# Optimization experiments

Hardware: AMD Instinct MI355X
Metric: run time of the kernel (lower is better)

Reference implementation:

```python
import jax, jax.numpy as jnp
import numpy as np
from jax import lax

B, CIN, COUT, H, W = 16, 320, 320, 64, 64
R, NUM_LORAS, LORA_STRIDE, SCALE, K = 4, 50, 4, 1.0, 3


def setup_inputs() -> dict:
    key = jax.random.key(0)
    k1, k2, k3, k4, k5, k6 = jax.random.split(key, 6)
    x = jax.random.normal(k1, (B, CIN, H, W), dtype=jnp.float32)
    lora_id = jax.random.randint(k2, (B,), 0, NUM_LORAS * LORA_STRIDE, dtype=jnp.int64)
    conv_w = jax.random.normal(k3, (COUT, CIN, K, K), dtype=jnp.float32) * (1.0 / np.sqrt(CIN * K * K))
    conv_b = jax.random.normal(k4, (COUT,), dtype=jnp.float32) * 0.01
    # stacked LoRA banks: down [L, r, Cin, 3, 3], up [L, Cout, r] (1x1 conv squeezed)
    down_w = jax.random.normal(k5, (NUM_LORAS, R, CIN, K, K), dtype=jnp.float32) * (1.0 / R)
    up_w = jax.random.normal(k6, (NUM_LORAS, COUT, R), dtype=jnp.float32) * 0.02
    return {"x": x, "conv_w": conv_w, "conv_b": conv_b, "down_w": down_w, "up_w": up_w, "lora_id": lora_id}


def _conv3x3(x, w):
    # x: [N, C, H, W], w: [O, C, 3, 3], stride 1, padding 1
    return lax.conv_general_dilated(x, w, (1, 1), [(1, 1), (1, 1)],
                                    dimension_numbers=("NCHW", "OIHW", "NCHW"))


def reference(x, conv_w, conv_b, down_w, up_w, lora_id):
    idx = lora_id // LORA_STRIDE                      # [B]
    active = (idx >= 0).astype(x.dtype)               # [B] mask; negative -> base conv only
    safe = jnp.clip(idx, 0, NUM_LORAS - 1)
    # base conv on full batch (dropout is identity at inference)
    base = _conv3x3(x, conv_w) + conv_b[None, :, None, None]  # [B, Cout, H, W]
    # per-sample gathered down conv (3x3), vmapped over batch (MoE-style dispatch)
    wd = down_w[safe]                                 # [B, r, Cin, 3, 3]
    down = jax.vmap(lambda xi, wi: _conv3x3(xi[None], wi)[0])(x, wd)  # [B, r, H, W]
    # per-sample 1x1 up conv as einsum with gathered up weights
    up = jnp.einsum("brhw,bor->bohw", down, up_w[safe])  # [B, Cout, H, W]
    return base + SCALE * up * active[:, None, None, None]
```

## Files before the change

kernel.cpp:

```cpp
#include <hip/hip_runtime.h>

typedef unsigned short ushort_t;
typedef unsigned int   uint_t;
typedef __attribute__((ext_vector_type(8))) short  short8;
typedef __attribute__((ext_vector_type(4))) float  float4v;
typedef __attribute__((ext_vector_type(4))) uint_t uint4v;
typedef __attribute__((ext_vector_type(2))) uint_t uint2v;

#define B_    16
#define CIN_  320
#define COUT_ 320
#define NLORA 50
#define R_    4
#define NCH   10

#define XCHUNK (66*66*32)
#define WCHUNK (9*COUT_*32)
#define DCHUNK (9*16*32)

#define WB16_OFF  44605440ULL
#define DWNE_OFF  46448640ULL
#define DOWN_OFF  47923200ULL

__device__ __forceinline__ ushort_t bf16rne(float f) {
  uint_t u = __float_as_uint(f);
  u = (u + 0x7FFFu + ((u >> 16) & 1u)) >> 16;
  return (ushort_t)u;
}

__device__ __forceinline__ void gld16(const ushort_t* g, ushort_t* l) {
  __builtin_amdgcn_global_load_lds(
      (const __attribute__((address_space(1))) void*)g,
      (__attribute__((address_space(3))) void*)l,
      16, 0, 0);
}

__device__ __forceinline__ void lora_idx(const void* lora, int b, int* l_out,
                                         float* act_out) {
  const int* p32 = (const int*)lora;
  bool odd0 = true;
  #pragma unroll
  for (int i = 1; i < 16; i += 2) odd0 = odd0 && (p32[i] == 0);
  long long raw = odd0 ? ((const long long*)lora)[b] : (long long)p32[b];
  long long idx = (raw >= 0) ? (raw >> 2) : -(((-raw) + 3) >> 2);
  *act_out = (idx >= 0) ? 1.0f : 0.0f;
  *l_out = (int)(idx < 0 ? 0 : (idx > (NLORA - 1) ? (NLORA - 1) : idx));
}

__global__ __launch_bounds__(256)
void pad_convert(const float* __restrict__ x, ushort_t* __restrict__ x_pad) {
  __shared__ float t[64][65];
  const int cc  = blockIdx.x;
  const int h   = blockIdx.y;
  const int b   = blockIdx.z;
  const int tid = threadIdx.x;
  #pragma unroll
  for (int it = 0; it < 4; ++it) {
    int idx = it * 256 + tid;
    int cl = idx >> 4, w4 = (idx & 15) * 4;
    float4v v = *(const float4v*)(x +
        (((size_t)(b * CIN_ + cc * 64 + cl)) * 64 + h) * 64 + w4);
    t[cl][w4] = v[0]; t[cl][w4 + 1] = v[1];
    t[cl][w4 + 2] = v[2]; t[cl][w4 + 3] = v[3];
  }
  __syncthreads();
  #pragma unroll
  for (int it = 0; it < 4; ++it) {
    int j  = it * 256 + tid;
    int cq = j & 15, wl = j >> 4;
    int cl = cq * 4;
    uint_t u0 = (uint_t)bf16rne(t[cl][wl])     | ((uint_t)bf16rne(t[cl + 1][wl]) << 16);
    uint_t u1 = (uint_t)bf16rne(t[cl + 2][wl]) | ((uint_t)bf16rne(t[cl + 3][wl]) << 16);
    int chunk = cc * 2 + (cl >> 5);
    uint2v u; u[0] = u0; u[1] = u1;
    *(uint2v*)(x_pad + (((size_t)(b * NCH + chunk) * 66 + (h + 1)) * 66 + (wl + 1)) * 32
               + (cl & 31)) = u;
  }
  if (h == 0) {
    #pragma unroll
    for (int s = 0; s < 2; ++s) {
      ushort_t* base = x_pad + (size_t)(b * NCH + cc * 2 + s) * XCHUNK;
      for (int g = tid; g < 528; g += 256) {
        int r = (g >= 264) ? 1 : 0;
        int g2 = g - r * 264;
        int col = g2 >> 2, qg = g2 & 3;
        *(uint4v*)(base + ((size_t)(r * 65) * 66 + col) * 32 + qg * 8) = (uint4v)0u;
      }
      for (int g = tid; g < 512; g += 256) {
        int row = 1 + (g >> 3);
        int col = ((g >> 2) & 1) * 65;
        int qg  = g & 3;
        *(uint4v*)(base + ((size_t)row * 66 + col) * 32 + qg * 8) = (uint4v)0u;
      }
    }
  }
}

__global__ __launch_bounds__(512)
void wconv(const float* __restrict__ conv_w, ushort_t* __restrict__ wb16) {
  int idx = blockIdx.x * 512 + threadIdx.x;
  int c5 = idx & 31;
  int o  = (idx >> 5) % COUT_;
  int rest = idx / (COUT_ * 32);
  int tap = rest % 9, chunk = rest / 9;
  wb16[idx] = bf16rne(conv_w[((size_t)o * CIN_ + chunk * 32 + c5) * 9 + tap]);
}

__global__ __launch_bounds__(512)
void dwnconv(const float* __restrict__ down_w, const void* __restrict__ lora,
             ushort_t* __restrict__ dwn_eff) {
  const int b = blockIdx.x;
  int l; float act;
  lora_idx(lora, b, &l, &act);
  ushort_t* dst = dwn_eff + (size_t)b * (NCH * DCHUNK);
  const float* src = down_w + (size_t)l * (R_ * CIN_ * 9);
  for (int it = 0; it < 90; ++it) {
    int idx = it * 512 + threadIdx.x;
    int c5 = idx & 31;
    int r  = (idx >> 5) & 15;
    int rest = idx >> 9;
    int tap = rest % 9, chunk = rest / 9;
    float v = (r < R_) ? act * src[((size_t)(r * CIN_) + chunk * 32 + c5) * 9 + tap]
                       : 0.0f;
    dst[idx] = bf16rne(v);
  }
}

#define LXG    1360
#define LXGP   1408
#define LWG    576
#define LTOTG  2048
#define LBUF_B (LTOTG * 16)

__global__ __launch_bounds__(512)
void lora_down(const ushort_t* __restrict__ x_pad, const ushort_t* __restrict__ dwn_eff,
               float* __restrict__ down) {
  __shared__ __align__(16) char smem[2 * LBUF_B];

  const int tid = threadIdx.x;
  const int lin = blockIdx.x;
  const int b   = lin >> 4;
  const int hw  = lin & 15;
  const int h0  = (hw & 7) * 8;
  const int w0  = (hw >> 3) * 32;

  const int wv = tid >> 6;
  const int la = tid & 15;
  const int q  = (tid >> 4) & 3;

  const ushort_t* psrc[4];
  int step[4];
  #pragma unroll
  for (int r = 0; r < 4; ++r) {
    int g = r * 512 + tid;
    if (g < LXGP) {
      int gx = (g < LXG) ? g : (LXG - 1);
      int qq = gx & 3, t = gx >> 2;
      int hh = t / 34, ww = t - hh * 34;
      psrc[r] = x_pad + (size_t)b * NCH * XCHUNK
              + (((h0 + hh) * 66 + (w0 + ww)) * 32 + (qq ^ ((ww >> 1) & 3)) * 8);
      step[r] = XCHUNK;
    } else {
      int gw = g - LXGP;
      if (gw > LWG - 1) gw = LWG - 1;
      int qq = gw & 3, t2 = gw >> 2;
      int rr = t2 & 15, tap = t2 >> 4;
      psrc[r] = dwn_eff + (size_t)b * NCH * DCHUNK
              + ((tap * 16 + rr) * 32 + (qq ^ ((rr >> 1) & 3)) * 8);
      step[r] = DCHUNK;
    }
  }

  const char* ax0[3]; const char* ax1[3];
  #pragma unroll
  for (int kw = 0; kw < 3; ++kw) {
    int base = (wv * 34 + la + kw) * 64 + (q ^ (((la + kw) >> 1) & 3)) * 16;
    ax0[kw] = smem + base;
    ax1[kw] = smem + LBUF_B + base;
  }
  const int bfb = 22528 + la * 64 + (q ^ ((la >> 1) & 3)) * 16;
  const char* aw0 = smem + bfb;
  const char* aw1 = smem + LBUF_B + bfb;

  float4v acc[2];
  acc[0] = (float4v)0.0f; acc[1] = (float4v)0.0f;

  auto STAGE = [&](int sel) {
    ushort_t* bufb = (ushort_t*)(smem + sel * LBUF_B);
    #pragma unroll
    for (int r = 0; r < 4; ++r) {
      gld16(psrc[r], bufb + (r * 512 + wv * 64) * 8);
      psrc[r] += step[r];
    }
  };

  auto PHASE = [&](const char* axA, const char* axB, const char* axC,
                   const char* aw, bool do_stage, int sel_next) {
    __builtin_amdgcn_s_barrier();
    if (do_stage) STAGE(sel_next);
    __builtin_amdgcn_sched_barrier(0);
    if (do_stage) asm volatile("s_waitcnt vmcnt(4)" ::: "memory");
    else          asm volatile("s_waitcnt vmcnt(0)" ::: "memory");
    __builtin_amdgcn_sched_barrier(0);
    __builtin_amdgcn_s_barrier();
    __builtin_amdgcn_s_setprio(1);
    #pragma unroll
    for (int tap = 0; tap < 9; ++tap) {
      const int kh = tap / 3, kw = tap - kh * 3;
      const char* ax = (kw == 0) ? axA : ((kw == 1) ? axB : axC);
      short8 bf = *(const short8*)(aw + tap * 1024);
      #pragma unroll
      for (int i = 0; i < 2; ++i) {
        short8 af = *(const short8*)(ax + kh * 2176 + i * 1024);
        acc[i] = __builtin_amdgcn_mfma_f32_16x16x32_bf16(af, bf, acc[i], 0, 0, 0);
      }
    }
    __builtin_amdgcn_s_setprio(0);
  };

  STAGE(0);
  #pragma unroll
  for (int tp = 0; tp < 5; ++tp) {
    PHASE(ax0[0], ax0[1], ax0[2], aw0, true,    1);
    PHASE(ax1[0], ax1[1], ax1[2], aw1, tp < 4,  0);
  }

  if (la < R_) {
    #pragma unroll
    for (int i = 0; i < 2; ++i)
      *(float4v*)(down + (((size_t)(b * R_ + la) * 64 + h0 + wv) * 64)
                  + w0 + i * 16 + q * 4) = acc[i];
  }
}

#define XG    1360
#define XGP   1408
#define WG    1152
#define TOTG  2560
#define BUF_B (TOTG * 16)

__global__ __launch_bounds__(512, 4)
void conv_main(const ushort_t* __restrict__ x_pad, const ushort_t* __restrict__ wb16,
               const float* __restrict__ conv_b, const float* __restrict__ up_w,
               const float* __restrict__ down, const void* __restrict__ lora,
               float* __restrict__ out) {
  __shared__ __align__(16) char smem[2 * BUF_B];

  const int tid = threadIdx.x;
  const int lin = blockIdx.x;
  const int wg  = (lin & 7) * 320 + (lin >> 3);
  const int b   = wg / 160;
  const int rem = wg - b * 160;
  const int o0  = (rem >> 4) * 32;
  const int hw  = rem & 15;
  const int h0  = (hw & 7) * 8;
  const int w0  = (hw >> 3) * 32;

  const int wv = tid >> 6;
  const int la = tid & 15;
  const int q  = (tid >> 4) & 3;

  const ushort_t* psrc[5];
  int step[5];
  #pragma unroll
  for (int r = 0; r < 5; ++r) {
    int g = r * 512 + tid;
    if (g < XGP) {
      int gx = (g < XG) ? g : (XG - 1);
      int qq = gx & 3, t = gx >> 2;
      int hh = t / 34, ww = t - hh * 34;
      psrc[r] = x_pad + (size_t)b * NCH * XCHUNK
              + (((h0 + hh) * 66 + (w0 + ww)) * 32 + (qq ^ ((ww >> 1) & 3)) * 8);
      step[r] = XCHUNK;
    } else {
      int gw = g - XGP;
      int qq = gw & 3, t2 = gw >> 2;
      int o = t2 & 31, tap = t2 >> 5;
      psrc[r] = wb16 + ((size_t)(tap * COUT_ + o0 + o) * 32 + (qq ^ ((o >> 1) & 3)) * 8);
      step[r] = WCHUNK;
    }
  }

  const char* ax0[3]; const char* ax1[3];
  #pragma unroll
  for (int kw = 0; kw < 3; ++kw) {
    int base = (wv * 34 + la + kw) * 64 + (q ^ (((la + kw) >> 1) & 3)) * 16;
    ax0[kw] = smem + base;
    ax1[kw] = smem + BUF_B + base;
  }
  const int bfb = 22528 + la * 64 + (q ^ ((la >> 1) & 3)) * 16;
  const char* aw0 = smem + bfb;
  const char* aw1 = smem + BUF_B + bfb;

  float4v acc[2][2];
  #pragma unroll
  for (int i = 0; i < 2; ++i)
    #pragma unroll
    for (int n = 0; n < 2; ++n) acc[i][n] = (float4v)0.0f;

  auto STAGE = [&](int sel) {
    ushort_t* bufb = (ushort_t*)(smem + sel * BUF_B);
    #pragma unroll
    for (int r = 0; r < 5; ++r) {
      gld16(psrc[r], bufb + (r * 512 + wv * 64) * 8);
      psrc[r] += step[r];
    }
  };

  auto PHASE = [&](const char* axA, const char* axB, const char* axC,
                   const char* aw, bool do_stage, int sel_next) {
    __builtin_amdgcn_s_barrier();
    if (do_stage) STAGE(sel_next);
    __builtin_amdgcn_sched_barrier(0);
    if (do_stage) asm volatile("s_waitcnt vmcnt(5)" ::: "memory");
    else          asm volatile("s_waitcnt vmcnt(0)" ::: "memory");
    __builtin_amdgcn_sched_barrier(0);
    __builtin_amdgcn_s_barrier();
    __builtin_amdgcn_s_setprio(1);
    #pragma unroll
    for (int tap = 0; tap < 9; ++tap) {
      const int kh = tap / 3, kw = tap - kh * 3;
      const char* ax = (kw == 0) ? axA : ((kw == 1) ? axB : axC);
      short8 bf0 = *(const short8*)(aw + tap * 2048);
      short8 bf1 = *(const short8*)(aw + tap * 2048 + 1024);
      #pragma unroll
      for (int i = 0; i < 2; ++i) {
        short8 af = *(const short8*)(ax + kh * 2176 + i * 1024);
        acc[i][0] = __builtin_amdgcn_mfma_f32_16x16x32_bf16(af, bf0, acc[i][0], 0, 0, 0);
        acc[i][1] = __builtin_amdgcn_mfma_f32_16x16x32_bf16(af, bf1, acc[i][1], 0, 0, 0);
      }
    }
    __builtin_amdgcn_s_setprio(0);
  };

  STAGE(0);
  #pragma unroll
  for (int tp = 0; tp < 5; ++tp) {
    PHASE(ax0[0], ax0[1], ax0[2], aw0, true,   1);
    PHASE(ax1[0], ax1[1], ax1[2], aw1, tp < 4, 0);
  }

  int l; float act;
  lora_idx(lora, b, &l, &act);
  const float* upb = up_w + (size_t)l * (COUT_ * R_);
  #pragma unroll
  for (int i = 0; i < 2; ++i) {
    float4v d[4];
    #pragma unroll
    for (int r = 0; r < 4; ++r)
      d[r] = *(const float4v*)(down + (((size_t)(b * R_ + r) * 64 + h0 + wv) * 64)
                               + w0 + i * 16 + q * 4);
    #pragma unroll
    for (int n = 0; n < 2; ++n) {
      const int o = o0 + n * 16 + la;
      float4v u = *(const float4v*)(upb + o * R_);
      float4v v = acc[i][n];
      v += conv_b[o];
      v += u[0] * d[0] + u[1] * d[1] + u[2] * d[2] + u[3] * d[3];
      *(float4v*)(out + (((size_t)(b * COUT_ + o) * 64 + h0 + wv) * 64)
                  + w0 + i * 16 + q * 4) = v;
    }
  }
}

extern "C" void kernel_launch(void* const* d_in, const int* in_sizes, int n_in,
                              void* d_out, int out_size, void* d_ws, size_t ws_size,
                              hipStream_t stream) {
  const float* x      = (const float*)d_in[0];
  const float* conv_w = (const float*)d_in[1];
  const float* conv_b = (const float*)d_in[2];
  const float* down_w = (const float*)d_in[3];
  const float* up_w   = (const float*)d_in[4];
  const void*  lora   = d_in[5];
  float* out = (float*)d_out;

  ushort_t* x_pad   = (ushort_t*)d_ws;
  ushort_t* wb16    = (ushort_t*)((char*)d_ws + WB16_OFF);
  ushort_t* dwn_eff = (ushort_t*)((char*)d_ws + DWNE_OFF);
  float*    down    = (float*)((char*)d_ws + DOWN_OFF);

  pad_convert<<<dim3(5, 64, 16), 256, 0, stream>>>(x, x_pad);
  wconv      <<<dim3(1800),      512, 0, stream>>>(conv_w, wb16);
  dwnconv    <<<dim3(16),        512, 0, stream>>>(down_w, lora, dwn_eff);
  lora_down  <<<dim3(256),       512, 0, stream>>>(x_pad, dwn_eff, down);
  conv_main  <<<dim3(2560),      512, 0, stream>>>(x_pad, wb16, conv_b, up_w,
                                                   down, lora, out);
}
```

Before: 302.0 us.

## Retile main conv to 64-channel full-width tiles using 32x32x16 MFMA

The main conv kernel now gives each workgroup 64 output channels over an 8-row, full 64-column strip, instead of 32 channels over an 8x32 patch. Each stage loads a 16-channel half chunk, so the loop runs 20 phases, and the inner loop uses 32x32x16 bf16 MFMAs with four 16-wide accumulators. Launching 640 blocks instead of 2560 cuts halo reloads and redundant weight traffic per output and raises MFMA arithmetic intensity. The cost is fewer blocks to fill the GPU, more barriers per K step, and a reworked epilogue indexing that must match the 32x32 accumulator layout.

```diff
diff --git a/kernel.cpp b/kernel.cpp
--- a/kernel.cpp
+++ b/kernel.cpp
@@ -2,10 +2,11 @@
 
 typedef unsigned short ushort_t;
 typedef unsigned int   uint_t;
-typedef __attribute__((ext_vector_type(8))) short  short8;
-typedef __attribute__((ext_vector_type(4))) float  float4v;
-typedef __attribute__((ext_vector_type(4))) uint_t uint4v;
-typedef __attribute__((ext_vector_type(2))) uint_t uint2v;
+typedef __attribute__((ext_vector_type(8)))  short  short8;
+typedef __attribute__((ext_vector_type(4)))  float  float4v;
+typedef __attribute__((ext_vector_type(16))) float  f32x16;
+typedef __attribute__((ext_vector_type(4)))  uint_t uint4v;
+typedef __attribute__((ext_vector_type(2)))  uint_t uint2v;
 
 #define B_    16
 #define CIN_  320
@@ -233,132 +234,140 @@
   }
 }
 
-#define XG    1360
-#define XGP   1408
-#define WG    1152
-#define TOTG  2560
-#define BUF_B (TOTG * 16)
-
 __global__ __launch_bounds__(512, 4)
 void conv_main(const ushort_t* __restrict__ x_pad, const ushort_t* __restrict__ wb16,
                const float* __restrict__ conv_b, const float* __restrict__ up_w,
                const float* __restrict__ down, const void* __restrict__ lora,
                float* __restrict__ out) {
-  __shared__ __align__(16) char smem[2 * BUF_B];
+  __shared__ __align__(16) char smem[81920];
 
   const int tid = threadIdx.x;
   const int lin = blockIdx.x;
-  const int wg  = (lin & 7) * 320 + (lin >> 3);
-  const int b   = wg / 160;
-  const int rem = wg - b * 160;
-  const int o0  = (rem >> 4) * 32;
-  const int hw  = rem & 15;
-  const int h0  = (hw & 7) * 8;
-  const int w0  = (hw >> 3) * 32;
-
-  const int wv = tid >> 6;
-  const int la = tid & 15;
-  const int q  = (tid >> 4) & 3;
+  const int wg  = (lin & 7) * 80 + (lin >> 3);
+  const int b   = wg / 40;
+  const int rr  = wg - b * 40;
+  const int ht  = rr / 5;
+  const int oc  = rr - ht * 5;
+  const int h0  = ht * 8;
+  const int o0  = oc * 64;
+
+  const int wv  = tid >> 6;
+  const int l31 = tid & 31;
+  const int l5  = (tid >> 5) & 1;
 
   const ushort_t* psrc[5];
-  int step[5];
+  int stepOdd[5];
   #pragma unroll
   for (int r = 0; r < 5; ++r) {
     int g = r * 512 + tid;
-    if (g < XGP) {
-      int gx = (g < XG) ? g : (XG - 1);
-      int qq = gx & 3, t = gx >> 2;
-      int hh = t / 34, ww = t - hh * 34;
-      psrc[r] = x_pad + (size_t)b * NCH * XCHUNK
-              + (((h0 + hh) * 66 + (w0 + ww)) * 32 + (qq ^ ((ww >> 1) & 3)) * 8);
-      step[r] = XCHUNK;
+    if (g > 2471) g = 2471;
+    if (g < 1320) {
+      int g2 = g & 1, t = g >> 1;
+      int hh = t / 66, ww = t - hh * 66;
+      int sq = g2 ^ ((ww >> 2) & 1);
+      psrc[r] = x_pad + (size_t)b * (NCH * XCHUNK)
+              + (((h0 + hh) * 66 + ww) * 32 + sq * 8);
+      stepOdd[r] = XCHUNK - 16;
     } else {
-      int gw = g - XGP;
-      int qq = gw & 3, t2 = gw >> 2;
-      int o = t2 & 31, tap = t2 >> 5;
-      psrc[r] = wb16 + ((size_t)(tap * COUT_ + o0 + o) * 32 + (qq ^ ((o >> 1) & 3)) * 8);
-      step[r] = WCHUNK;
-    }
-  }
-
-  const char* ax0[3]; const char* ax1[3];
-  #pragma unroll
-  for (int kw = 0; kw < 3; ++kw) {
-    int base = (wv * 34 + la + kw) * 64 + (q ^ (((la + kw) >> 1) & 3)) * 16;
-    ax0[kw] = smem + base;
-    ax1[kw] = smem + BUF_B + base;
-  }
-  const int bfb = 22528 + la * 64 + (q ^ ((la >> 1) & 3)) * 16;
-  const char* aw0 = smem + bfb;
-  const char* aw1 = smem + BUF_B + bfb;
-
-  float4v acc[2][2];
-  #pragma unroll
-  for (int i = 0; i < 2; ++i)
-    #pragma unroll
-    for (int n = 0; n < 2; ++n) acc[i][n] = (float4v)0.0f;
-
-  auto STAGE = [&](int sel) {
-    ushort_t* bufb = (ushort_t*)(smem + sel * BUF_B);
+      int gw = g - 1320;
+      int g2 = gw & 1, t2 = gw >> 1;
+      int o = t2 & 63, tap = t2 >> 6;
+      int sq = g2 ^ ((o >> 2) & 1);
+      psrc[r] = wb16 + (((size_t)tap * COUT_ + o0 + o) * 32 + sq * 8);
+      stepOdd[r] = WCHUNK - 16;
+    }
+  }
+
+  int axo[3];
+  #pragma unroll
+  for (int kw = 0; kw < 3; ++kw)
+    axo[kw] = (wv * 66 + l31 + kw) * 32 + (l5 ^ (((l31 + kw) >> 2) & 1)) * 16;
+  const int awo = 21120 + l31 * 32 + (l5 ^ ((l31 >> 2) & 1)) * 16;
+
+  f32x16 acc00 = (f32x16)0.0f, acc01 = (f32x16)0.0f;
+  f32x16 acc10 = (f32x16)0.0f, acc11 = (f32x16)0.0f;
+
+  auto STAGE = [&](int sel, bool evenAdv) {
+    ushort_t* bb = (ushort_t*)(smem + sel * 40960);
     #pragma unroll
     for (int r = 0; r < 5; ++r) {
-      gld16(psrc[r], bufb + (r * 512 + wv * 64) * 8);
-      psrc[r] += step[r];
+      gld16(psrc[r], bb + (r * 512 + wv * 64) * 8);
+      psrc[r] += evenAdv ? 16 : stepOdd[r];
     }
   };
 
-  auto PHASE = [&](const char* axA, const char* axB, const char* axC,
-                   const char* aw, bool do_stage, int sel_next) {
+  auto PHASE = [&](int rb, bool stage, bool evenAdv) {
+    asm volatile("" ::: "memory");
     __builtin_amdgcn_s_barrier();
-    if (do_stage) STAGE(sel_next);
+    if (stage) STAGE(rb ^ 1, evenAdv);
     __builtin_amdgcn_sched_barrier(0);
-    if (do_stage) asm volatile("s_waitcnt vmcnt(5)" ::: "memory");
-    else          asm volatile("s_waitcnt vmcnt(0)" ::: "memory");
+    if (stage) asm volatile("s_waitcnt vmcnt(5)" ::: "memory");
+    else       asm volatile("s_waitcnt vmcnt(0)" ::: "memory");
     __builtin_amdgcn_sched_barrier(0);
     __builtin_amdgcn_s_barrier();
+    asm volatile("" ::: "memory");
+    const char* bb = smem + rb * 40960;
     __builtin_amdgcn_s_setprio(1);
     #pragma unroll
     for (int tap = 0; tap < 9; ++tap) {
       const int kh = tap / 3, kw = tap - kh * 3;
-      const char* ax = (kw == 0) ? axA : ((kw == 1) ? axB : axC);
-      short8 bf0 = *(const short8*)(aw + tap * 2048);
-      short8 bf1 = *(const short8*)(aw + tap * 2048 + 1024);
-      #pragma unroll
-      for (int i = 0; i < 2; ++i) {
-        short8 af = *(const short8*)(ax + kh * 2176 + i * 1024);
-        acc[i][0] = __builtin_amdgcn_mfma_f32_16x16x32_bf16(af, bf0, acc[i][0], 0, 0, 0);
-        acc[i][1] = __builtin_amdgcn_mfma_f32_16x16x32_bf16(af, bf1, acc[i][1], 0, 0, 0);
-      }
+      short8 bf0 = *(const short8*)(bb + awo + tap * 2048);
+      short8 bf1 = *(const short8*)(bb + awo + tap * 2048 + 1024);
+      short8 af0 = *(const short8*)(bb + axo[kw] + kh * 2112);
+      short8 af1 = *(const short8*)(bb + axo[kw] + kh * 2112 + 1024);
+      acc00 = __builtin_amdgcn_mfma_f32_32x32x16_bf16(af0, bf0, acc00, 0, 0, 0);
+      acc01 = __builtin_amdgcn_mfma_f32_32x32x16_bf16(af0, bf1, acc01, 0, 0, 0);
+      acc10 = __builtin_amdgcn_mfma_f32_32x32x16_bf16(af1, bf0, acc10, 0, 0, 0);
+      acc11 = __builtin_amdgcn_mfma_f32_32x32x16_bf16(af1, bf1, acc11, 0, 0, 0);
     }
     __builtin_amdgcn_s_setprio(0);
   };
 
-  STAGE(0);
-  #pragma unroll
-  for (int tp = 0; tp < 5; ++tp) {
-    PHASE(ax0[0], ax0[1], ax0[2], aw0, true,   1);
-    PHASE(ax1[0], ax1[1], ax1[2], aw1, tp < 4, 0);
+  STAGE(0, true);
+  for (int tp = 0; tp < 10; ++tp) {
+    PHASE(0, true,    false);
+    PHASE(1, tp < 9,  true);
   }
 
   int l; float act;
   lora_idx(lora, b, &l, &act);
   const float* upb = up_w + (size_t)l * (COUT_ * R_);
+  const int h = h0 + wv;
+  const int row4 = l5 * 4;
+  const float* dbase = down + (size_t)b * (R_ * 4096) + h * 64;
+  float4v u0 = *(const float4v*)(upb + (o0 + l31) * R_);
+  float4v u1 = *(const float4v*)(upb + (o0 + 32 + l31) * R_);
+  const float bias0 = conv_b[o0 + l31];
+  const float bias1 = conv_b[o0 + 32 + l31];
+  float* ob0 = out + (((size_t)(b * COUT_ + o0 + l31)) * 64 + h) * 64;
+  float* ob1 = out + (((size_t)(b * COUT_ + o0 + 32 + l31)) * 64 + h) * 64;
   #pragma unroll
   for (int i = 0; i < 2; ++i) {
-    float4v d[4];
-    #pragma unroll
-    for (int r = 0; r < 4; ++r)
-      d[r] = *(const float4v*)(down + (((size_t)(b * R_ + r) * 64 + h0 + wv) * 64)
-                               + w0 + i * 16 + q * 4);
-    #pragma unroll
-    for (int n = 0; n < 2; ++n) {
-      const int o = o0 + n * 16 + la;
-      float4v u = *(const float4v*)(upb + o * R_);
-      float4v v = acc[i][n];
-      v += conv_b[o];
-      v += u[0] * d[0] + u[1] * d[1] + u[2] * d[2] + u[3] * d[3];
-      *(float4v*)(out + (((size_t)(b * COUT_ + o) * 64 + h0 + wv) * 64)
-                  + w0 + i * 16 + q * 4) = v;
+    #pragma unroll
+    for (int qd = 0; qd < 4; ++qd) {
+      const int wl = i * 32 + qd * 8 + row4;
+      float4v d0 = *(const float4v*)(dbase + 0 * 4096 + wl);
+      float4v d1 = *(const float4v*)(dbase + 1 * 4096 + wl);
+      float4v d2 = *(const float4v*)(dbase + 2 * 4096 + wl);
+      float4v d3 = *(const float4v*)(dbase + 3 * 4096 + wl);
+      {
+        const f32x16& A = (i == 0) ? acc00 : acc10;
+        float4v v;
+        v[0] = A[qd * 4 + 0]; v[1] = A[qd * 4 + 1];
+        v[2] = A[qd * 4 + 2]; v[3] = A[qd * 4 + 3];
+        v += bias0;
+        v += u0[0] * d0 + u0[1] * d1 + u0[2] * d2 + u0[3] * d3;
+        *(float4v*)(ob0 + wl) = v;
+      }
+      {
+        const f32x16& A = (i == 0) ? acc01 : acc11;
+        float4v v;
+        v[0] = A[qd * 4 + 0]; v[1] = A[qd * 4 + 1];
+        v[2] = A[qd * 4 + 2]; v[3] = A[qd * 4 + 3];
+        v += bias1;
+        v += u1[0] * d0 + u1[1] * d1 + u1[2] * d2 + u1[3] * d3;
+        *(float4v*)(ob1 + wl) = v;
+      }
     }
   }
 }
@@ -383,6 +392,6 @@
   wconv      <<<dim3(1800),      512, 0, stream>>>(conv_w, wb16);
   dwnconv    <<<dim3(16),        512, 0, stream>>>(down_w, lora, dwn_eff);
   lora_down  <<<dim3(256),       512, 0, stream>>>(x_pad, dwn_eff, down);
-  conv_main  <<<dim3(2560),      512, 0, stream>>>(x_pad, wb16, conv_b, up_w,
+  conv_main  <<<dim3(640),       512, 0, stream>>>(x_pad, wb16, conv_b, up_w,
                                                    down, lora, out);
 }
```

New measurement: 320.6 us. 1.06x slower.
